# Kernel optimization log

Hardware: AMD Instinct MI355X
Metric: run time of the kernel (lower is better)

The kernel has to match this reference:

```python
import jax, jax.numpy as jnp
import numpy as np

GAMMA = 0.99
LAM = 0.95
CLIP = 0.2
VALUE_COEFF = 0.5
ENTROPY_COEFF = 0.01
T = 500_000
S = 128
A = 16


def _mlp(x, W1, b1, W2, b2, W3, b3):
    h = jax.nn.relu(x @ W1 + b1)
    h = jax.nn.relu(h @ W2 + b2)
    return h @ W3 + b3


def setup_inputs() -> dict:
    key = jax.random.key(0)
    ks = jax.random.split(key, 12)
    states = jax.random.normal(ks[0], (T, S), dtype=jnp.float32)
    next_states = jax.random.normal(ks[1], (T, S), dtype=jnp.float32)
    rewards = jax.random.normal(ks[2], (T,), dtype=jnp.float32)
    dones = (jax.random.uniform(ks[3], (T,)) < 0.01).astype(jnp.float32)
    actions = jax.random.randint(ks[4], (T,), 0, A)
    # old log-probs of taken actions (valid log-probabilities)
    old_logp = jnp.log(jax.random.uniform(ks[5], (T,), minval=1e-3, maxval=1.0))

    def lin(k, fan_in, fan_out):
        lim = 1.0 / np.sqrt(fan_in)
        return jax.random.uniform(k, (fan_in, fan_out), minval=-lim, maxval=lim, dtype=jnp.float32)

    return {
        'states': states, 'next_states': next_states, 'rewards': rewards,
        'dones': dones, 'actions': actions, 'old_logp': old_logp,
        'aW1': lin(ks[6], S, 64), 'ab1': jnp.zeros((64,), jnp.float32),
        'aW2': lin(ks[7], 64, 64), 'ab2': jnp.zeros((64,), jnp.float32),
        'aW3': lin(ks[8], 64, A), 'ab3': jnp.zeros((A,), jnp.float32),
        'cW1': lin(ks[9], S, 64), 'cb1': jnp.zeros((64,), jnp.float32),
        'cW2': lin(ks[10], 64, 64), 'cb2': jnp.zeros((64,), jnp.float32),
        'cW3': lin(ks[11], 64, 1), 'cb3': jnp.zeros((1,), jnp.float32),
    }


def reference(states, next_states, rewards, dones, actions, old_logp,
              aW1, ab1, aW2, ab2, aW3, ab3,
              cW1, cb1, cW2, cb2, cW3, cb3):
    # ---- critic values and TD deltas ----
    values = _mlp(states, cW1, cb1, cW2, cb2, cW3, cb3)[:, 0]        # [T]
    next_values = _mlp(next_states, cW1, cb1, cW2, cb2, cW3, cb3)[:, 0]
    not_done = 1.0 - dones
    deltas = rewards + GAMMA * next_values * not_done - values       # [T]

    # ---- GAE: reverse-time linear recurrence a_t = c_t * a_{t+1} + d_t ----
    coef = GAMMA * LAM * not_done

    def step(carry, cd):
        c, d = cd
        a = c * carry + d
        return a, a

    _, advantages = jax.lax.scan(step, jnp.float32(0.0), (coef, deltas), reverse=True)
    returns = advantages + values
    adv_n = (advantages - advantages.mean()) / (jnp.std(advantages, ddof=1) + 1e-8)

    # ---- actor: clipped surrogate ----
    probs = jax.nn.softmax(_mlp(states, aW1, ab1, aW2, ab2, aW3, ab3), axis=-1)  # [T, A]
    logp = jnp.log(jnp.take_along_axis(probs, actions[:, None], axis=1))[:, 0]   # [T]
    ratios = jnp.exp(logp - old_logp)
    surr1 = ratios * adv_n
    surr2 = jnp.clip(ratios, 1.0 - CLIP, 1.0 + CLIP) * adv_n
    actor_loss = -jnp.minimum(surr1, surr2).mean()

    # ---- critic MSE loss ----
    critic_loss = jnp.mean((values - returns) ** 2)

    # ---- entropy bonus ----
    entropy_loss = jnp.mean(-jnp.sum(probs * jnp.log(probs + 1e-8), axis=-1))

    total_loss = actor_loss + VALUE_COEFF * critic_loss - ENTROPY_COEFF * entropy_loss
    return jnp.stack([total_loss, actor_loss, critic_loss, entropy_loss])
```

## Files before the change

kernel.cpp:

```cpp
#include <hip/hip_runtime.h>
#include <hip/hip_bf16.h>

#define T_N 500000
#define NTILE 31250
#define NCHUNK 4096
#define CHUNKL 128
#define NPART 1024

typedef __attribute__((ext_vector_type(8))) short short8v;
typedef __attribute__((ext_vector_type(4))) float float4v;

__device__ __forceinline__ short f2bf(float f) {
    __hip_bfloat16 b = __float2bfloat16(f);
    return *reinterpret_cast<short*>(&b);
}

__device__ __forceinline__ short8v cvt8(const float4 a, const float4 b) {
    short8v r;
    r[0] = f2bf(a.x); r[1] = f2bf(a.y); r[2] = f2bf(a.z); r[3] = f2bf(a.w);
    r[4] = f2bf(b.x); r[5] = f2bf(b.y); r[6] = f2bf(b.z); r[7] = f2bf(b.w);
    return r;
}

#define FC1 0
#define FA1 16
#define FC2 32
#define FA2 40
#define FA3 48
#define NFRAG 50

__global__ __launch_bounds__(64) void k_pack(
    const float* __restrict__ cW1, const float* __restrict__ aW1,
    const float* __restrict__ cW2, const float* __restrict__ aW2,
    const float* __restrict__ aW3, short8v* __restrict__ packed)
{
    const int f = blockIdx.x, l = threadIdx.x;
    const int g = l >> 4, col = l & 15;
    const float* W; int s, c, ncol;
    if (f < FA1)      { W = cW1; s = f >> 2;         c = f & 3;         ncol = 64; }
    else if (f < FC2) { W = aW1; s = (f - FA1) >> 2; c = (f - FA1) & 3; ncol = 64; }
    else if (f < FA2) { W = cW2; s = (f - FC2) >> 2; c = (f - FC2) & 3; ncol = 64; }
    else if (f < FA3) { W = aW2; s = (f - FA2) >> 2; c = (f - FA2) & 3; ncol = 64; }
    else              { W = aW3; s = f - FA3;        c = 0;             ncol = 16; }
    short8v frag;
    #pragma unroll
    for (int j = 0; j < 8; ++j) {
        int k = s * 32 + g * 8 + j;
        frag[j] = f2bf(W[k * ncol + c * 16 + col]);
    }
    packed[f * 64 + l] = frag;
}

__device__ __forceinline__ void store_h(short (*hb)[68], const float4v* acc, int g, int q) {
    #pragma unroll
    for (int c = 0; c < 4; ++c)
        #pragma unroll
        for (int r = 0; r < 4; ++r)
            hb[g * 4 + r][c * 16 + q] = f2bf(fmaxf(acc[c][r], 0.f));
}

__global__ __launch_bounds__(256, 4) void k_mlp(
    const float* __restrict__ states, const float* __restrict__ next_states,
    const float* __restrict__ rewards, const float* __restrict__ dones,
    const int* __restrict__ actions, const float* __restrict__ old_logp,
    const short8v* __restrict__ pk,
    const float* __restrict__ cb1, const float* __restrict__ ab1,
    const float* __restrict__ cb2, const float* __restrict__ ab2,
    const float* __restrict__ ab3,
    const float* __restrict__ cW3, const float* __restrict__ cb3,
    float* __restrict__ delta_o, float* __restrict__ coef_o,
    float* __restrict__ ratio_o, float* __restrict__ ent_o)
{
    __shared__ __align__(16) short hlds[4][2][16][68];
    const int wv = threadIdx.x >> 6, l = threadIdx.x & 63;
    const int g = l >> 4, q = l & 15;
    const int tile = blockIdx.x * 4 + wv;
    if (tile >= NTILE) return;
    const long long r0 = (long long)tile * 16;
    short (*h0)[68] = hlds[wv][0];
    short (*h1)[68] = hlds[wv][1];

    const float* xs = states + (r0 + q) * 128 + g * 8;
    const float* xn = next_states + (r0 + q) * 128 + g * 8;
    float4 rs[8], rn[8];
    #pragma unroll
    for (int s = 0; s < 4; ++s) {
        rs[2 * s]     = *reinterpret_cast<const float4*>(xs + s * 32);
        rs[2 * s + 1] = *reinterpret_cast<const float4*>(xs + s * 32 + 4);
    }
    #pragma unroll
    for (int s = 0; s < 4; ++s) {
        rn[2 * s]     = *reinterpret_cast<const float4*>(xn + s * 32);
        rn[2 * s + 1] = *reinterpret_cast<const float4*>(xn + s * 32 + 4);
    }
    short8v sa[4], na[4];
    #pragma unroll
    for (int s = 0; s < 4; ++s) sa[s] = cvt8(rs[2 * s], rs[2 * s + 1]);
    #pragma unroll
    for (int s = 0; s < 4; ++s) na[s] = cvt8(rn[2 * s], rn[2 * s + 1]);

    float4v accC[4], accN[4];
    #pragma unroll
    for (int c = 0; c < 4; ++c) {
        float b = cb1[c * 16 + q];
        accC[c] = (float4v){b, b, b, b};
        accN[c] = accC[c];
    }
    #pragma unroll
    for (int s = 0; s < 4; ++s) {
        #pragma unroll
        for (int c = 0; c < 4; ++c) {
            short8v w = pk[(FC1 + s * 4 + c) * 64 + l];
            accC[c] = __builtin_amdgcn_mfma_f32_16x16x32_bf16(sa[s], w, accC[c], 0, 0, 0);
            accN[c] = __builtin_amdgcn_mfma_f32_16x16x32_bf16(na[s], w, accN[c], 0, 0, 0);
        }
    }
    store_h(h0, accC, g, q);
    store_h(h1, accN, g, q);

    float4v c2C[4], c2N[4];
    #pragma unroll
    for (int c = 0; c < 4; ++c) {
        float b = cb2[c * 16 + q];
        c2C[c] = (float4v){b, b, b, b};
        c2N[c] = c2C[c];
    }
    #pragma unroll
    for (int s = 0; s < 2; ++s) {
        short8v aC = *reinterpret_cast<const short8v*>(&h0[q][s * 32 + g * 8]);
        short8v aN = *reinterpret_cast<const short8v*>(&h1[q][s * 32 + g * 8]);
        #pragma unroll
        for (int c = 0; c < 4; ++c) {
            short8v w = pk[(FC2 + s * 4 + c) * 64 + l];
            c2C[c] = __builtin_amdgcn_mfma_f32_16x16x32_bf16(aC, w, c2C[c], 0, 0, 0);
            c2N[c] = __builtin_amdgcn_mfma_f32_16x16x32_bf16(aN, w, c2N[c], 0, 0, 0);
        }
    }
    float vr[4] = {0.f, 0.f, 0.f, 0.f}, nr[4] = {0.f, 0.f, 0.f, 0.f};
    #pragma unroll
    for (int c = 0; c < 4; ++c) {
        float w3 = cW3[c * 16 + q];
        #pragma unroll
        for (int r = 0; r < 4; ++r) {
            vr[r] = fmaf(fmaxf(c2C[c][r], 0.f), w3, vr[r]);
            nr[r] = fmaf(fmaxf(c2N[c][r], 0.f), w3, nr[r]);
        }
    }
    #pragma unroll
    for (int o = 1; o < 16; o <<= 1)
        #pragma unroll
        for (int r = 0; r < 4; ++r) {
            vr[r] += __shfl_xor(vr[r], o);
            nr[r] += __shfl_xor(nr[r], o);
        }
    const float cb3v = cb3[0];
    float v[4], nv[4];
    #pragma unroll
    for (int r = 0; r < 4; ++r) { v[r] = vr[r] + cb3v; nv[r] = nr[r] + cb3v; }

    float4v aA[4];
    #pragma unroll
    for (int c = 0; c < 4; ++c) { float b = ab1[c * 16 + q]; aA[c] = (float4v){b, b, b, b}; }
    #pragma unroll
    for (int s = 0; s < 4; ++s)
        #pragma unroll
        for (int c = 0; c < 4; ++c)
            aA[c] = __builtin_amdgcn_mfma_f32_16x16x32_bf16(sa[s], pk[(FA1 + s * 4 + c) * 64 + l], aA[c], 0, 0, 0);
    store_h(h0, aA, g, q);

    float4v a2[4];
    #pragma unroll
    for (int c = 0; c < 4; ++c) { float b = ab2[c * 16 + q]; a2[c] = (float4v){b, b, b, b}; }
    #pragma unroll
    for (int s = 0; s < 2; ++s) {
        short8v aa = *reinterpret_cast<const short8v*>(&h0[q][s * 32 + g * 8]);
        #pragma unroll
        for (int c = 0; c < 4; ++c)
            a2[c] = __builtin_amdgcn_mfma_f32_16x16x32_bf16(aa, pk[(FA2 + s * 4 + c) * 64 + l], a2[c], 0, 0, 0);
    }
    store_h(h1, a2, g, q);

    const float b3 = ab3[q];
    float4v a3 = (float4v){b3, b3, b3, b3};
    #pragma unroll
    for (int s = 0; s < 2; ++s) {
        short8v aa = *reinterpret_cast<const short8v*>(&h1[q][s * 32 + g * 8]);
        a3 = __builtin_amdgcn_mfma_f32_16x16x32_bf16(aa, pk[(FA3 + s) * 64 + l], a3, 0, 0, 0);
    }

    float lg[4], mx[4], pe[4], se[4], tt[4], ent[4], logp[4];
    #pragma unroll
    for (int r = 0; r < 4; ++r) { lg[r] = a3[r]; mx[r] = lg[r]; }
    #pragma unroll
    for (int o = 1; o < 16; o <<= 1)
        #pragma unroll
        for (int r = 0; r < 4; ++r) mx[r] = fmaxf(mx[r], __shfl_xor(mx[r], o));
    #pragma unroll
    for (int r = 0; r < 4; ++r) {
        pe[r] = __expf(lg[r] - mx[r]);
        se[r] = pe[r];
        tt[r] = pe[r] * lg[r];
    }
    #pragma unroll
    for (int o = 1; o < 16; o <<= 1)
        #pragma unroll
        for (int r = 0; r < 4; ++r) {
            se[r] += __shfl_xor(se[r], o);
            tt[r] += __shfl_xor(tt[r], o);
        }
    const int4 av = *reinterpret_cast<const int4*>(&actions[r0 + g * 4]);
    const int act[4] = {av.x, av.y, av.z, av.w};
    #pragma unroll
    for (int r = 0; r < 4; ++r) {
        float ls = __logf(se[r]);
        ent[r] = mx[r] + ls - tt[r] / se[r];
        float sel = __shfl(lg[r], (l & 48) | act[r]);
        logp[r] = sel - mx[r] - ls;
    }

    if (q == 0) {
        const long long rb = r0 + g * 4;
        const float4 rw = *reinterpret_cast<const float4*>(&rewards[rb]);
        const float4 dn = *reinterpret_cast<const float4*>(&dones[rb]);
        const float4 ol = *reinterpret_cast<const float4*>(&old_logp[rb]);
        const float rwv[4] = {rw.x, rw.y, rw.z, rw.w};
        const float dnv[4] = {dn.x, dn.y, dn.z, dn.w};
        const float olv[4] = {ol.x, ol.y, ol.z, ol.w};
        const float GL = 0.99f * 0.95f;
        float dl[4], cf[4], rt[4];
        #pragma unroll
        for (int r = 0; r < 4; ++r) {
            float nd = 1.f - dnv[r];
            dl[r] = fmaf(0.99f * nd, nv[r], rwv[r]) - v[r];
            cf[r] = GL * nd;
            rt[r] = __expf(logp[r] - olv[r]);
        }
        float4 t;
        t.x = dl[0]; t.y = dl[1]; t.z = dl[2]; t.w = dl[3];
        *reinterpret_cast<float4*>(&delta_o[rb]) = t;
        t.x = cf[0]; t.y = cf[1]; t.z = cf[2]; t.w = cf[3];
        *reinterpret_cast<float4*>(&coef_o[rb]) = t;
        t.x = rt[0]; t.y = rt[1]; t.z = rt[2]; t.w = rt[3];
        *reinterpret_cast<float4*>(&ratio_o[rb]) = t;
        t.x = ent[0]; t.y = ent[1]; t.z = ent[2]; t.w = ent[3];
        *reinterpret_cast<float4*>(&ent_o[rb]) = t;
    }
}

__global__ __launch_bounds__(256) void k_gae_chunk(
    const float* __restrict__ coef, const float* __restrict__ delta,
    float* __restrict__ P, float* __restrict__ Q)
{
    const int c = blockIdx.x * 256 + threadIdx.x;
    const long long lo = (long long)c * CHUNKL;
    float p = 1.f, a = 0.f;
    if (lo < T_N) {
        const int n = (int)((T_N - lo < CHUNKL) ? (T_N - lo) : CHUNKL);
        for (int j = (n >> 2) - 1; j >= 0; --j) {
            float4 cfv = *reinterpret_cast<const float4*>(&coef[lo + 4 * j]);
            float4 dlv = *reinterpret_cast<const float4*>(&delta[lo + 4 * j]);
            a = fmaf(cfv.w, a, dlv.w);
            a = fmaf(cfv.z, a, dlv.z);
            a = fmaf(cfv.y, a, dlv.y);
            a = fmaf(cfv.x, a, dlv.x);
            p *= cfv.x * cfv.y * cfv.z * cfv.w;
        }
    }
    P[c] = p; Q[c] = a;
}

__global__ __launch_bounds__(1024) void k_gae_scan(
    const float* __restrict__ P, const float* __restrict__ Q,
    float* __restrict__ carry)
{
    __shared__ float sp[1024], sq[1024];
    const int t = threadIdx.x, b = t * 4;
    float p = P[b + 3], q = Q[b + 3];
    #pragma unroll
    for (int c = 2; c >= 0; --c) {
        float pc = P[b + c], qc = Q[b + c];
        q = fmaf(pc, q, qc);
        p = pc * p;
    }
    sp[t] = p; sq[t] = q;
    __syncthreads();
    for (int d = 1; d < 1024; d <<= 1) {
        float pp = sp[t], qq = sq[t];
        float p2 = 1.f, q2 = 0.f;
        const bool has = (t + d) < 1024;
        if (has) { p2 = sp[t + d]; q2 = sq[t + d]; }
        __syncthreads();
        if (has) { sp[t] = pp * p2; sq[t] = fmaf(pp, q2, qq); }
        __syncthreads();
    }
    float x = (t + 1 < 1024) ? sq[t + 1] : 0.f;
    #pragma unroll
    for (int c = 3; c >= 0; --c) {
        carry[b + c] = x;
        x = fmaf(P[b + c], x, Q[b + c]);
    }
}

__global__ __launch_bounds__(256) void k_gae_apply(
    const float* __restrict__ coef, const float* __restrict__ delta,
    const float* __restrict__ carry, float* __restrict__ adv,
    float* __restrict__ part)
{
    const int c = blockIdx.x * 256 + threadIdx.x;
    const long long lo = (long long)c * CHUNKL;
    float s = 0.f, s2 = 0.f;
    if (lo < T_N) {
        const int n = (int)((T_N - lo < CHUNKL) ? (T_N - lo) : CHUNKL);
        float a = carry[c];
        for (int j = (n >> 2) - 1; j >= 0; --j) {
            float4 cfv = *reinterpret_cast<const float4*>(&coef[lo + 4 * j]);
            float4 dlv = *reinterpret_cast<const float4*>(&delta[lo + 4 * j]);
            float a3 = fmaf(cfv.w, a, dlv.w);
            float a2v = fmaf(cfv.z, a3, dlv.z);
            float a1 = fmaf(cfv.y, a2v, dlv.y);
            float a0 = fmaf(cfv.x, a1, dlv.x);
            float4 o; o.x = a0; o.y = a1; o.z = a2v; o.w = a3;
            *reinterpret_cast<float4*>(&adv[lo + 4 * j]) = o;
            a = a0;
            s += a0 + a1 + a2v + a3;
            s2 += a0 * a0 + a1 * a1 + a2v * a2v + a3 * a3;
        }
    }
    #pragma unroll
    for (int o = 32; o > 0; o >>= 1) { s += __shfl_down(s, o); s2 += __shfl_down(s2, o); }
    __shared__ float l0[4], l1[4];
    const int wv = threadIdx.x >> 6, ln = threadIdx.x & 63;
    if (ln == 0) { l0[wv] = s; l1[wv] = s2; }
    __syncthreads();
    if (threadIdx.x == 0) {
        part[blockIdx.x * 2]     = l0[0] + l0[1] + l0[2] + l0[3];
        part[blockIdx.x * 2 + 1] = l1[0] + l1[1] + l1[2] + l1[3];
    }
}

__global__ __launch_bounds__(256) void k_actor(
    const float* __restrict__ adv, const float* __restrict__ ratio,
    const float* __restrict__ ent, const float* __restrict__ part,
    float* __restrict__ part4)
{
    __shared__ float st[2];
    if (threadIdx.x == 0) {
        float S = 0.f, S2 = 0.f;
        #pragma unroll
        for (int i = 0; i < 16; ++i) { S += part[2 * i]; S2 += part[2 * i + 1]; }
        const float Tf = (float)T_N;
        float mean = S / Tf;
        float var = (S2 - S * S / Tf) / (Tf - 1.f);
        st[0] = mean;
        st[1] = 1.f / (sqrtf(fmaxf(var, 0.f)) + 1e-8f);
    }
    __syncthreads();
    const float mean = st[0], isd = st[1];
    float sm = 0.f, se = 0.f;
    for (long long i = (long long)blockIdx.x * 256 + threadIdx.x; i < T_N;
         i += (long long)gridDim.x * 256) {
        float an = (adv[i] - mean) * isd;
        float rt = ratio[i];
        float s1 = rt * an;
        float s2v = fminf(fmaxf(rt, 0.8f), 1.2f) * an;
        sm += fminf(s1, s2v);
        se += ent[i];
    }
    #pragma unroll
    for (int o = 32; o > 0; o >>= 1) { sm += __shfl_down(sm, o); se += __shfl_down(se, o); }
    __shared__ float l0[4], l1[4];
    const int wv = threadIdx.x >> 6, ln = threadIdx.x & 63;
    if (ln == 0) { l0[wv] = sm; l1[wv] = se; }
    __syncthreads();
    if (threadIdx.x == 0) {
        part4[blockIdx.x * 2]     = l0[0] + l0[1] + l0[2] + l0[3];
        part4[blockIdx.x * 2 + 1] = l1[0] + l1[1] + l1[2] + l1[3];
    }
}

__global__ __launch_bounds__(1024) void k_final(
    const float* __restrict__ part4, const float* __restrict__ part,
    float* __restrict__ out)
{
    const int t = threadIdx.x;
    float sm = part4[t * 2], se = part4[t * 2 + 1];
    #pragma unroll
    for (int o = 32; o > 0; o >>= 1) { sm += __shfl_down(sm, o); se += __shfl_down(se, o); }
    __shared__ float l0[16], l1[16];
    const int wv = t >> 6, ln = t & 63;
    if (ln == 0) { l0[wv] = sm; l1[wv] = se; }
    __syncthreads();
    if (t == 0) {
        float SM = 0.f, SE = 0.f;
        #pragma unroll
        for (int i = 0; i < 16; ++i) { SM += l0[i]; SE += l1[i]; }
        float S2 = 0.f;
        #pragma unroll
        for (int i = 0; i < 16; ++i) S2 += part[2 * i + 1];
        const float Tf = (float)T_N;
        float actor_loss = -SM / Tf;
        float ent_loss = SE / Tf;
        float critic_loss = S2 / Tf;
        float total = actor_loss + 0.5f * critic_loss - 0.01f * ent_loss;
        out[0] = total; out[1] = actor_loss; out[2] = critic_loss; out[3] = ent_loss;
    }
}

extern "C" void kernel_launch(void* const* d_in, const int* in_sizes, int n_in,
                              void* d_out, int out_size, void* d_ws, size_t ws_size,
                              hipStream_t stream) {
    (void)in_sizes; (void)n_in; (void)out_size; (void)ws_size;
    const float* states      = (const float*)d_in[0];
    const float* next_states = (const float*)d_in[1];
    const float* rewards     = (const float*)d_in[2];
    const float* dones       = (const float*)d_in[3];
    const int*   actions     = (const int*)d_in[4];
    const float* old_logp    = (const float*)d_in[5];
    const float* aW1 = (const float*)d_in[6];  const float* ab1 = (const float*)d_in[7];
    const float* aW2 = (const float*)d_in[8];  const float* ab2 = (const float*)d_in[9];
    const float* aW3 = (const float*)d_in[10]; const float* ab3 = (const float*)d_in[11];
    const float* cW1 = (const float*)d_in[12]; const float* cb1 = (const float*)d_in[13];
    const float* cW2 = (const float*)d_in[14]; const float* cb2 = (const float*)d_in[15];
    const float* cW3 = (const float*)d_in[16]; const float* cb3 = (const float*)d_in[17];
    float* out = (float*)d_out;

    float* ws = (float*)d_ws;
    float* delta = ws;
    float* coef  = ws + 1 * (size_t)T_N;
    float* ratio = ws + 2 * (size_t)T_N;
    float* entb  = ws + 3 * (size_t)T_N;
    float* adv   = ws + 4 * (size_t)T_N;
    float* P     = ws + 5 * (size_t)T_N;
    float* Q     = P + NCHUNK;
    float* carry = Q + NCHUNK;
    float* part  = carry + NCHUNK;
    float* part4 = part + 32;
    short8v* packed = (short8v*)(part4 + 2048);

    k_pack<<<NFRAG, 64, 0, stream>>>(cW1, aW1, cW2, aW2, aW3, packed);
    k_mlp<<<(NTILE + 3) / 4, 256, 0, stream>>>(
        states, next_states, rewards, dones, actions, old_logp, packed,
        cb1, ab1, cb2, ab2, ab3, cW3, cb3, delta, coef, ratio, entb);
    k_gae_chunk<<<NCHUNK / 256, 256, 0, stream>>>(coef, delta, P, Q);
    k_gae_scan<<<1, 1024, 0, stream>>>(P, Q, carry);
    k_gae_apply<<<NCHUNK / 256, 256, 0, stream>>>(coef, delta, carry, adv, part);
    k_actor<<<NPART, 256, 0, stream>>>(adv, ratio, entb, part, part4);
    k_final<<<1, 1024, 0, stream>>>(part4, part, out);
}
```

Baseline: 214.7 us.

## Make MLP kernel persistent with register prefetch of next tile's inputs

Turns the MLP kernel into a persistent grid of 768 blocks where each wave loops over tiles with stride NWAVES. Inside the loop it issues the global loads for the next tile's states and next_states into registers while the current tile's MFMA work runs, aiming to hide HBM latency behind compute. The occupancy hint in launch_bounds is dropped, and the prefetch registers raise register pressure, which may lower occupancy.

```diff
diff --git a/kernel.cpp b/kernel.cpp
--- a/kernel.cpp
+++ b/kernel.cpp
@@ -3,6 +3,8 @@
 
 #define T_N 500000
 #define NTILE 31250
+#define NBLK 768
+#define NWAVES (NBLK * 4)
 #define NCHUNK 4096
 #define CHUNKL 128
 #define NPART 1024
@@ -59,7 +61,7 @@
             hb[g * 4 + r][c * 16 + q] = f2bf(fmaxf(acc[c][r], 0.f));
 }
 
-__global__ __launch_bounds__(256, 4) void k_mlp(
+__global__ __launch_bounds__(256) void k_mlp(
     const float* __restrict__ states, const float* __restrict__ next_states,
     const float* __restrict__ rewards, const float* __restrict__ dones,
     const int* __restrict__ actions, const float* __restrict__ old_logp,
@@ -74,176 +76,197 @@
     __shared__ __align__(16) short hlds[4][2][16][68];
     const int wv = threadIdx.x >> 6, l = threadIdx.x & 63;
     const int g = l >> 4, q = l & 15;
-    const int tile = blockIdx.x * 4 + wv;
-    if (tile >= NTILE) return;
-    const long long r0 = (long long)tile * 16;
     short (*h0)[68] = hlds[wv][0];
     short (*h1)[68] = hlds[wv][1];
 
-    const float* xs = states + (r0 + q) * 128 + g * 8;
-    const float* xn = next_states + (r0 + q) * 128 + g * 8;
+    int tile = blockIdx.x * 4 + wv;
+    if (tile >= NTILE) return;
+
     float4 rs[8], rn[8];
-    #pragma unroll
-    for (int s = 0; s < 4; ++s) {
-        rs[2 * s]     = *reinterpret_cast<const float4*>(xs + s * 32);
-        rs[2 * s + 1] = *reinterpret_cast<const float4*>(xs + s * 32 + 4);
-    }
-    #pragma unroll
-    for (int s = 0; s < 4; ++s) {
-        rn[2 * s]     = *reinterpret_cast<const float4*>(xn + s * 32);
-        rn[2 * s + 1] = *reinterpret_cast<const float4*>(xn + s * 32 + 4);
-    }
-    short8v sa[4], na[4];
-    #pragma unroll
-    for (int s = 0; s < 4; ++s) sa[s] = cvt8(rs[2 * s], rs[2 * s + 1]);
-    #pragma unroll
-    for (int s = 0; s < 4; ++s) na[s] = cvt8(rn[2 * s], rn[2 * s + 1]);
-
-    float4v accC[4], accN[4];
-    #pragma unroll
-    for (int c = 0; c < 4; ++c) {
-        float b = cb1[c * 16 + q];
-        accC[c] = (float4v){b, b, b, b};
-        accN[c] = accC[c];
-    }
-    #pragma unroll
-    for (int s = 0; s < 4; ++s) {
+    {
+        const float* xs = states + ((long long)tile * 16 + q) * 128 + g * 8;
+        const float* xn = next_states + ((long long)tile * 16 + q) * 128 + g * 8;
+        #pragma unroll
+        for (int s = 0; s < 4; ++s) {
+            rs[2 * s]     = *reinterpret_cast<const float4*>(xs + s * 32);
+            rs[2 * s + 1] = *reinterpret_cast<const float4*>(xs + s * 32 + 4);
+            rn[2 * s]     = *reinterpret_cast<const float4*>(xn + s * 32);
+            rn[2 * s + 1] = *reinterpret_cast<const float4*>(xn + s * 32 + 4);
+        }
+    }
+
+    while (true) {
+        const int next = tile + NWAVES;
+        const long long r0 = (long long)tile * 16;
+
+        short8v sa[4], na[4];
+        #pragma unroll
+        for (int s = 0; s < 4; ++s) {
+            sa[s] = cvt8(rs[2 * s], rs[2 * s + 1]);
+            na[s] = cvt8(rn[2 * s], rn[2 * s + 1]);
+        }
+
+        if (next < NTILE) {
+            const float* xs = states + ((long long)next * 16 + q) * 128 + g * 8;
+            const float* xn = next_states + ((long long)next * 16 + q) * 128 + g * 8;
+            #pragma unroll
+            for (int s = 0; s < 4; ++s) {
+                rs[2 * s]     = *reinterpret_cast<const float4*>(xs + s * 32);
+                rs[2 * s + 1] = *reinterpret_cast<const float4*>(xs + s * 32 + 4);
+                rn[2 * s]     = *reinterpret_cast<const float4*>(xn + s * 32);
+                rn[2 * s + 1] = *reinterpret_cast<const float4*>(xn + s * 32 + 4);
+            }
+        }
+
+        float4v accC[4], accN[4];
         #pragma unroll
         for (int c = 0; c < 4; ++c) {
-            short8v w = pk[(FC1 + s * 4 + c) * 64 + l];
-            accC[c] = __builtin_amdgcn_mfma_f32_16x16x32_bf16(sa[s], w, accC[c], 0, 0, 0);
-            accN[c] = __builtin_amdgcn_mfma_f32_16x16x32_bf16(na[s], w, accN[c], 0, 0, 0);
-        }
-    }
-    store_h(h0, accC, g, q);
-    store_h(h1, accN, g, q);
-
-    float4v c2C[4], c2N[4];
-    #pragma unroll
-    for (int c = 0; c < 4; ++c) {
-        float b = cb2[c * 16 + q];
-        c2C[c] = (float4v){b, b, b, b};
-        c2N[c] = c2C[c];
-    }
-    #pragma unroll
-    for (int s = 0; s < 2; ++s) {
-        short8v aC = *reinterpret_cast<const short8v*>(&h0[q][s * 32 + g * 8]);
-        short8v aN = *reinterpret_cast<const short8v*>(&h1[q][s * 32 + g * 8]);
+            float b = cb1[c * 16 + q];
+            accC[c] = (float4v){b, b, b, b};
+            accN[c] = accC[c];
+        }
+        #pragma unroll
+        for (int s = 0; s < 4; ++s) {
+            #pragma unroll
+            for (int c = 0; c < 4; ++c) {
+                short8v w = pk[(FC1 + s * 4 + c) * 64 + l];
+                accC[c] = __builtin_amdgcn_mfma_f32_16x16x32_bf16(sa[s], w, accC[c], 0, 0, 0);
+                accN[c] = __builtin_amdgcn_mfma_f32_16x16x32_bf16(na[s], w, accN[c], 0, 0, 0);
+            }
+        }
+        store_h(h0, accC, g, q);
+        store_h(h1, accN, g, q);
+
+        float4v c2C[4], c2N[4];
         #pragma unroll
         for (int c = 0; c < 4; ++c) {
-            short8v w = pk[(FC2 + s * 4 + c) * 64 + l];
-            c2C[c] = __builtin_amdgcn_mfma_f32_16x16x32_bf16(aC, w, c2C[c], 0, 0, 0);
-            c2N[c] = __builtin_amdgcn_mfma_f32_16x16x32_bf16(aN, w, c2N[c], 0, 0, 0);
-        }
-    }
-    float vr[4] = {0.f, 0.f, 0.f, 0.f}, nr[4] = {0.f, 0.f, 0.f, 0.f};
-    #pragma unroll
-    for (int c = 0; c < 4; ++c) {
-        float w3 = cW3[c * 16 + q];
+            float b = cb2[c * 16 + q];
+            c2C[c] = (float4v){b, b, b, b};
+            c2N[c] = c2C[c];
+        }
+        #pragma unroll
+        for (int s = 0; s < 2; ++s) {
+            short8v aC = *reinterpret_cast<const short8v*>(&h0[q][s * 32 + g * 8]);
+            short8v aN = *reinterpret_cast<const short8v*>(&h1[q][s * 32 + g * 8]);
+            #pragma unroll
+            for (int c = 0; c < 4; ++c) {
+                short8v w = pk[(FC2 + s * 4 + c) * 64 + l];
+                c2C[c] = __builtin_amdgcn_mfma_f32_16x16x32_bf16(aC, w, c2C[c], 0, 0, 0);
+                c2N[c] = __builtin_amdgcn_mfma_f32_16x16x32_bf16(aN, w, c2N[c], 0, 0, 0);
+            }
+        }
+        float vr[4] = {0.f, 0.f, 0.f, 0.f}, nr[4] = {0.f, 0.f, 0.f, 0.f};
+        #pragma unroll
+        for (int c = 0; c < 4; ++c) {
+            float w3 = cW3[c * 16 + q];
+            #pragma unroll
+            for (int r = 0; r < 4; ++r) {
+                vr[r] = fmaf(fmaxf(c2C[c][r], 0.f), w3, vr[r]);
+                nr[r] = fmaf(fmaxf(c2N[c][r], 0.f), w3, nr[r]);
+            }
+        }
+        #pragma unroll
+        for (int o = 1; o < 16; o <<= 1)
+            #pragma unroll
+            for (int r = 0; r < 4; ++r) {
+                vr[r] += __shfl_xor(vr[r], o);
+                nr[r] += __shfl_xor(nr[r], o);
+            }
+        const float cb3v = cb3[0];
+        float v[4], nv[4];
+        #pragma unroll
+        for (int r = 0; r < 4; ++r) { v[r] = vr[r] + cb3v; nv[r] = nr[r] + cb3v; }
+
+        float4v aA[4];
+        #pragma unroll
+        for (int c = 0; c < 4; ++c) { float b = ab1[c * 16 + q]; aA[c] = (float4v){b, b, b, b}; }
+        #pragma unroll
+        for (int s = 0; s < 4; ++s)
+            #pragma unroll
+            for (int c = 0; c < 4; ++c)
+                aA[c] = __builtin_amdgcn_mfma_f32_16x16x32_bf16(sa[s], pk[(FA1 + s * 4 + c) * 64 + l], aA[c], 0, 0, 0);
+        store_h(h0, aA, g, q);
+
+        float4v a2[4];
+        #pragma unroll
+        for (int c = 0; c < 4; ++c) { float b = ab2[c * 16 + q]; a2[c] = (float4v){b, b, b, b}; }
+        #pragma unroll
+        for (int s = 0; s < 2; ++s) {
+            short8v aa = *reinterpret_cast<const short8v*>(&h0[q][s * 32 + g * 8]);
+            #pragma unroll
+            for (int c = 0; c < 4; ++c)
+                a2[c] = __builtin_amdgcn_mfma_f32_16x16x32_bf16(aa, pk[(FA2 + s * 4 + c) * 64 + l], a2[c], 0, 0, 0);
+        }
+        store_h(h1, a2, g, q);
+
+        const float b3 = ab3[q];
+        float4v a3 = (float4v){b3, b3, b3, b3};
+        #pragma unroll
+        for (int s = 0; s < 2; ++s) {
+            short8v aa = *reinterpret_cast<const short8v*>(&h1[q][s * 32 + g * 8]);
+            a3 = __builtin_amdgcn_mfma_f32_16x16x32_bf16(aa, pk[(FA3 + s) * 64 + l], a3, 0, 0, 0);
+        }
+
+        float lg[4], mx[4], pe[4], se[4], tt[4], ent[4], logp[4];
+        #pragma unroll
+        for (int r = 0; r < 4; ++r) { lg[r] = a3[r]; mx[r] = lg[r]; }
+        #pragma unroll
+        for (int o = 1; o < 16; o <<= 1)
+            #pragma unroll
+            for (int r = 0; r < 4; ++r) mx[r] = fmaxf(mx[r], __shfl_xor(mx[r], o));
         #pragma unroll
         for (int r = 0; r < 4; ++r) {
-            vr[r] = fmaf(fmaxf(c2C[c][r], 0.f), w3, vr[r]);
-            nr[r] = fmaf(fmaxf(c2N[c][r], 0.f), w3, nr[r]);
-        }
-    }
-    #pragma unroll
-    for (int o = 1; o < 16; o <<= 1)
+            pe[r] = __expf(lg[r] - mx[r]);
+            se[r] = pe[r];
+            tt[r] = pe[r] * lg[r];
+        }
+        #pragma unroll
+        for (int o = 1; o < 16; o <<= 1)
+            #pragma unroll
+            for (int r = 0; r < 4; ++r) {
+                se[r] += __shfl_xor(se[r], o);
+                tt[r] += __shfl_xor(tt[r], o);
+            }
+        const int4 av = *reinterpret_cast<const int4*>(&actions[r0 + g * 4]);
+        const int act[4] = {av.x, av.y, av.z, av.w};
         #pragma unroll
         for (int r = 0; r < 4; ++r) {
-            vr[r] += __shfl_xor(vr[r], o);
-            nr[r] += __shfl_xor(nr[r], o);
-        }
-    const float cb3v = cb3[0];
-    float v[4], nv[4];
-    #pragma unroll
-    for (int r = 0; r < 4; ++r) { v[r] = vr[r] + cb3v; nv[r] = nr[r] + cb3v; }
-
-    float4v aA[4];
-    #pragma unroll
-    for (int c = 0; c < 4; ++c) { float b = ab1[c * 16 + q]; aA[c] = (float4v){b, b, b, b}; }
-    #pragma unroll
-    for (int s = 0; s < 4; ++s)
-        #pragma unroll
-        for (int c = 0; c < 4; ++c)
-            aA[c] = __builtin_amdgcn_mfma_f32_16x16x32_bf16(sa[s], pk[(FA1 + s * 4 + c) * 64 + l], aA[c], 0, 0, 0);
-    store_h(h0, aA, g, q);
-
-    float4v a2[4];
-    #pragma unroll
-    for (int c = 0; c < 4; ++c) { float b = ab2[c * 16 + q]; a2[c] = (float4v){b, b, b, b}; }
-    #pragma unroll
-    for (int s = 0; s < 2; ++s) {
-        short8v aa = *reinterpret_cast<const short8v*>(&h0[q][s * 32 + g * 8]);
-        #pragma unroll
-        for (int c = 0; c < 4; ++c)
-            a2[c] = __builtin_amdgcn_mfma_f32_16x16x32_bf16(aa, pk[(FA2 + s * 4 + c) * 64 + l], a2[c], 0, 0, 0);
-    }
-    store_h(h1, a2, g, q);
-
-    const float b3 = ab3[q];
-    float4v a3 = (float4v){b3, b3, b3, b3};
-    #pragma unroll
-    for (int s = 0; s < 2; ++s) {
-        short8v aa = *reinterpret_cast<const short8v*>(&h1[q][s * 32 + g * 8]);
-        a3 = __builtin_amdgcn_mfma_f32_16x16x32_bf16(aa, pk[(FA3 + s) * 64 + l], a3, 0, 0, 0);
-    }
-
-    float lg[4], mx[4], pe[4], se[4], tt[4], ent[4], logp[4];
-    #pragma unroll
-    for (int r = 0; r < 4; ++r) { lg[r] = a3[r]; mx[r] = lg[r]; }
-    #pragma unroll
-    for (int o = 1; o < 16; o <<= 1)
-        #pragma unroll
-        for (int r = 0; r < 4; ++r) mx[r] = fmaxf(mx[r], __shfl_xor(mx[r], o));
-    #pragma unroll
-    for (int r = 0; r < 4; ++r) {
-        pe[r] = __expf(lg[r] - mx[r]);
-        se[r] = pe[r];
-        tt[r] = pe[r] * lg[r];
-    }
-    #pragma unroll
-    for (int o = 1; o < 16; o <<= 1)
-        #pragma unroll
-        for (int r = 0; r < 4; ++r) {
-            se[r] += __shfl_xor(se[r], o);
-            tt[r] += __shfl_xor(tt[r], o);
-        }
-    const int4 av = *reinterpret_cast<const int4*>(&actions[r0 + g * 4]);
-    const int act[4] = {av.x, av.y, av.z, av.w};
-    #pragma unroll
-    for (int r = 0; r < 4; ++r) {
-        float ls = __logf(se[r]);
-        ent[r] = mx[r] + ls - tt[r] / se[r];
-        float sel = __shfl(lg[r], (l & 48) | act[r]);
-        logp[r] = sel - mx[r] - ls;
-    }
-
-    if (q == 0) {
-        const long long rb = r0 + g * 4;
-        const float4 rw = *reinterpret_cast<const float4*>(&rewards[rb]);
-        const float4 dn = *reinterpret_cast<const float4*>(&dones[rb]);
-        const float4 ol = *reinterpret_cast<const float4*>(&old_logp[rb]);
-        const float rwv[4] = {rw.x, rw.y, rw.z, rw.w};
-        const float dnv[4] = {dn.x, dn.y, dn.z, dn.w};
-        const float olv[4] = {ol.x, ol.y, ol.z, ol.w};
-        const float GL = 0.99f * 0.95f;
-        float dl[4], cf[4], rt[4];
-        #pragma unroll
-        for (int r = 0; r < 4; ++r) {
-            float nd = 1.f - dnv[r];
-            dl[r] = fmaf(0.99f * nd, nv[r], rwv[r]) - v[r];
-            cf[r] = GL * nd;
-            rt[r] = __expf(logp[r] - olv[r]);
-        }
-        float4 t;
-        t.x = dl[0]; t.y = dl[1]; t.z = dl[2]; t.w = dl[3];
-        *reinterpret_cast<float4*>(&delta_o[rb]) = t;
-        t.x = cf[0]; t.y = cf[1]; t.z = cf[2]; t.w = cf[3];
-        *reinterpret_cast<float4*>(&coef_o[rb]) = t;
-        t.x = rt[0]; t.y = rt[1]; t.z = rt[2]; t.w = rt[3];
-        *reinterpret_cast<float4*>(&ratio_o[rb]) = t;
-        t.x = ent[0]; t.y = ent[1]; t.z = ent[2]; t.w = ent[3];
-        *reinterpret_cast<float4*>(&ent_o[rb]) = t;
+            float ls = __logf(se[r]);
+            ent[r] = mx[r] + ls - tt[r] / se[r];
+            float sel = __shfl(lg[r], (l & 48) | act[r]);
+            logp[r] = sel - mx[r] - ls;
+        }
+
+        if (q == 0) {
+            const long long rb = r0 + g * 4;
+            const float4 rw = *reinterpret_cast<const float4*>(&rewards[rb]);
+            const float4 dn = *reinterpret_cast<const float4*>(&dones[rb]);
+            const float4 ol = *reinterpret_cast<const float4*>(&old_logp[rb]);
+            const float rwv[4] = {rw.x, rw.y, rw.z, rw.w};
+            const float dnv[4] = {dn.x, dn.y, dn.z, dn.w};
+            const float olv[4] = {ol.x, ol.y, ol.z, ol.w};
+            const float GL = 0.99f * 0.95f;
+            float dl[4], cf[4], rt[4];
+            #pragma unroll
+            for (int r = 0; r < 4; ++r) {
+                float nd = 1.f - dnv[r];
+                dl[r] = fmaf(0.99f * nd, nv[r], rwv[r]) - v[r];
+                cf[r] = GL * nd;
+                rt[r] = __expf(logp[r] - olv[r]);
+            }
+            float4 t;
+            t.x = dl[0]; t.y = dl[1]; t.z = dl[2]; t.w = dl[3];
+            *reinterpret_cast<float4*>(&delta_o[rb]) = t;
+            t.x = cf[0]; t.y = cf[1]; t.z = cf[2]; t.w = cf[3];
+            *reinterpret_cast<float4*>(&coef_o[rb]) = t;
+            t.x = rt[0]; t.y = rt[1]; t.z = rt[2]; t.w = rt[3];
+            *reinterpret_cast<float4*>(&ratio_o[rb]) = t;
+            t.x = ent[0]; t.y = ent[1]; t.z = ent[2]; t.w = ent[3];
+            *reinterpret_cast<float4*>(&ent_o[rb]) = t;
+        }
+
+        if (next >= NTILE) break;
+        tile = next;
     }
 }
 
@@ -438,7 +461,7 @@
     short8v* packed = (short8v*)(part4 + 2048);
 
     k_pack<<<NFRAG, 64, 0, stream>>>(cW1, aW1, cW2, aW2, aW3, packed);
-    k_mlp<<<(NTILE + 3) / 4, 256, 0, stream>>>(
+    k_mlp<<<NBLK, 256, 0, stream>>>(
         states, next_states, rewards, dones, actions, old_logp, packed,
         cb1, ab1, cb2, ab2, ab3, cW3, cb3, delta, coef, ratio, entb);
     k_gae_chunk<<<NCHUNK / 256, 256, 0, stream>>>(coef, delta, P, Q);
```

New measurement: 225.7 us. +5.1%, slower.
